# Optimization experiments

Hardware: AMD Instinct MI355X
Metric: run time of the kernel (lower is better)

Reference implementation:

```python
import jax, jax.numpy as jnp
import numpy as np


def _maxpool2(t):
    # 2x2x2 max pool, stride 2. t: [B, C, D, H, W]
    B, C, D, H, W = t.shape
    return t.reshape(B, C, D // 2, 2, H // 2, 2, W // 2, 2).max(axis=(3, 5, 7))


def setup_inputs() -> dict:
    key = jax.random.key(0)
    ks = jax.random.split(key, 5)
    ch = 64
    B, D, H, W = 2, 32, 32, 32
    x = jax.random.normal(ks[0], (B, ch, D, H, W), dtype=jnp.float32)
    # 1x1x1 conv weights (out_ch, in_ch), Kaiming-ish scale
    w_theta = jax.random.normal(ks[1], (ch // 8, ch), dtype=jnp.float32) / np.sqrt(ch)
    w_phi = jax.random.normal(ks[2], (ch // 8, ch), dtype=jnp.float32) / np.sqrt(ch)
    w_g = jax.random.normal(ks[3], (ch // 2, ch), dtype=jnp.float32) / np.sqrt(ch)
    w_o = jax.random.normal(ks[4], (ch, ch // 2), dtype=jnp.float32) / np.sqrt(ch // 2)
    gamma = jnp.ones((), dtype=jnp.float32)  # original inits at 0; 1 gives nontrivial output
    return {"x": x, "w_theta": w_theta, "w_phi": w_phi, "w_g": w_g, "w_o": w_o, "gamma": gamma}


def reference(x, w_theta, w_phi, w_g, w_o, gamma):
    B, C, D, H, W = x.shape
    N = D * H * W
    M = N // 8
    xf = x.reshape(B, C, N)  # [B, C, N]
    # 1x1x1 convs = channel matmuls
    theta = jnp.einsum('oc,bcn->bon', w_theta, xf)                     # [B, C//8, N]
    phi = _maxpool2(jnp.einsum('oc,bcn->bon', w_phi, xf).reshape(B, C // 8, D, H, W)).reshape(B, C // 8, M)
    g = _maxpool2(jnp.einsum('oc,bcn->bon', w_g, xf).reshape(B, C // 2, D, H, W)).reshape(B, C // 2, M)
    # unscaled attention: softmax over keys (M)
    beta = jax.nn.softmax(jnp.einsum('bcn,bcm->bnm', theta, phi), axis=-1)  # [B, N, M]
    o = jnp.einsum('bcm,bnm->bcn', g, beta)                                 # [B, C//2, N]
    out = gamma * jnp.einsum('oc,bcn->bon', w_o, o).reshape(B, C, D, H, W) + x
    return out
```

## Files before the change

### kernel.cpp

```cpp
#include <hip/hip_runtime.h>
#include <cstdint>
#include <cstddef>

typedef __attribute__((ext_vector_type(4))) short short4v;
typedef __attribute__((ext_vector_type(4))) float float4v;

#define C_IN  64
#define NB    2
#define NPTS  32768
#define MPTS  4096
#define LOG2E 1.44269504088896340736f
#define KT    64
#define NTILE (MPTS / KT)
#define QTILES (NPTS / 32)

__device__ __forceinline__ unsigned short f2bf_rne(float f) {
  unsigned int u = __builtin_bit_cast(unsigned int, f);
  u += 0x7fffu + ((u >> 16) & 1u);
  return (unsigned short)(u >> 16);
}

__device__ __forceinline__ short4v pack_bf16_trunc(float a0, float a1, float a2, float a3) {
  unsigned int u0 = __builtin_amdgcn_perm(__builtin_bit_cast(unsigned int, a1),
                                          __builtin_bit_cast(unsigned int, a0), 0x07060302u);
  unsigned int u1 = __builtin_amdgcn_perm(__builtin_bit_cast(unsigned int, a3),
                                          __builtin_bit_cast(unsigned int, a2), 0x07060302u);
  union { unsigned int u[2]; short4v s; } r;
  r.u[0] = u0; r.u[1] = u1;
  return r.s;
}

__device__ __forceinline__ short4v pack_bf16_rne(float a0, float a1, float a2, float a3) {
  short4v s;
  s[0] = (short)f2bf_rne(a0); s[1] = (short)f2bf_rne(a1);
  s[2] = (short)f2bf_rne(a2); s[3] = (short)f2bf_rne(a3);
  return s;
}

__device__ __forceinline__ void gl_lds16(const unsigned short* g, unsigned short* l) {
  __builtin_amdgcn_global_load_lds(
      (const __attribute__((address_space(1))) void*)g,
      (__attribute__((address_space(3))) void*)l, 16, 0, 0);
}


__device__ void pool_body(int idx, const float* __restrict__ x,
                          const float* __restrict__ w_phi,
                          const float* __restrict__ w_g,
                          unsigned short* __restrict__ phi_f,
                          unsigned short* __restrict__ g_f) {
  int b = idx >> 15;
  int rem = idx & 32767;
  int m = rem >> 3, pos = rem & 7;
  int md = m >> 8, mh = (m >> 4) & 15, mw = m & 15;
  int dd = pos >> 2, hh = (pos >> 1) & 1, ww = pos & 1;
  int n = (md * 2 + dd) * 1024 + (mh * 2 + hh) * 32 + (mw * 2 + ww);
  const float* xb = x + (size_t)b * C_IN * NPTS + n;

  float acc[40];
#pragma unroll
  for (int o = 0; o < 40; ++o) acc[o] = 0.f;

#pragma unroll 4
  for (int cc = 0; cc < C_IN; ++cc) {
    float xv = xb[(size_t)cc * NPTS];
#pragma unroll
    for (int o = 0; o < 8; ++o)  acc[o] = fmaf(w_phi[o * C_IN + cc], xv, acc[o]);
#pragma unroll
    for (int o = 0; o < 32; ++o) acc[8 + o] = fmaf(w_g[o * C_IN + cc], xv, acc[8 + o]);
  }

#pragma unroll
  for (int o = 0; o < 40; ++o) {
    float v = acc[o];
    v = fmaxf(v, __shfl_xor(v, 1, 64));
    v = fmaxf(v, __shfl_xor(v, 2, 64));
    v = fmaxf(v, __shfl_xor(v, 4, 64));
    acc[o] = v;
  }

  if (pos == 0) {
    int kt16 = m >> 4, kr = m & 15;
    size_t fb = ((size_t)b * 256 + kt16) * 256;
#pragma unroll
    for (int g2 = 0; g2 < 2; ++g2) {
      unsigned int u0 = (unsigned int)f2bf_rne(acc[g2 * 4 + 0] * LOG2E)
                      | ((unsigned int)f2bf_rne(acc[g2 * 4 + 1] * LOG2E) << 16);
      unsigned int u1 = (unsigned int)f2bf_rne(acc[g2 * 4 + 2] * LOG2E)
                      | ((unsigned int)f2bf_rne(acc[g2 * 4 + 3] * LOG2E) << 16);
      *(uint2*)&phi_f[fb + (g2 * 16 + kr) * 4] = make_uint2(u0, u1);
    }
#pragma unroll
    for (int g2 = 2; g2 < 4; ++g2) {
      *(uint2*)&phi_f[fb + (g2 * 16 + kr) * 4] = make_uint2(0u, 0u);
    }
#pragma unroll
    for (int o = 0; o < 32; ++o) {
      int half = o >> 4, c15 = o & 15;
      size_t base = (((size_t)b * 256 + kt16) * 2 + half) * 256;
      g_f[base + ((kr >> 2) * 16 + c15) * 4 + (kr & 3)] = f2bf_rne(acc[8 + o]);
    }
  }
}

__device__ void theta_body(int idx, const float* __restrict__ x,
                           const float* __restrict__ w_theta,
                           unsigned short* __restrict__ theta_pad) {
  int b = idx >> 15, n = idx & 32767;
  const float* xb = x + (size_t)b * C_IN * NPTS + n;
  float t[8];
#pragma unroll
  for (int o = 0; o < 8; ++o) t[o] = 0.f;
#pragma unroll 4
  for (int cc = 0; cc < C_IN; ++cc) {
    float xv = xb[(size_t)cc * NPTS];
#pragma unroll
    for (int o = 0; o < 8; ++o) t[o] = fmaf(w_theta[o * C_IN + cc], xv, t[o]);
  }
  unsigned int w0 = (unsigned int)f2bf_rne(t[0]) | ((unsigned int)f2bf_rne(t[1]) << 16);
  unsigned int w1 = (unsigned int)f2bf_rne(t[2]) | ((unsigned int)f2bf_rne(t[3]) << 16);
  unsigned int w2 = (unsigned int)f2bf_rne(t[4]) | ((unsigned int)f2bf_rne(t[5]) << 16);
  unsigned int w3 = (unsigned int)f2bf_rne(t[6]) | ((unsigned int)f2bf_rne(t[7]) << 16);
  uint4* dst = (uint4*)(theta_pad + ((size_t)idx << 4));
  dst[0] = make_uint4(w0, w1, w2, w3);
  dst[1] = make_uint4(0u, 0u, 0u, 0u);
}

__global__ __launch_bounds__(256) void prep_fused(
    const float* __restrict__ x, const float* __restrict__ w_theta,
    const float* __restrict__ w_phi, const float* __restrict__ w_g,
    unsigned short* __restrict__ theta_pad,
    unsigned short* __restrict__ phi_f,
    unsigned short* __restrict__ g_f) {
  int gb = blockIdx.x;
  if (gb < 256) {
    pool_body(gb * 256 + threadIdx.x, x, w_phi, w_g, phi_f, g_f);
  } else {
    theta_body((gb - 256) * 256 + threadIdx.x, x, w_theta, theta_pad);
  }
}

template <int KS>
__global__ __launch_bounds__(256) void attn_split_nl(
    const unsigned short* __restrict__ theta_pad,
    const unsigned short* __restrict__ phi_f,
    const unsigned short* __restrict__ g_f,
    float4v* __restrict__ opart,
    float* __restrict__ lbuf) {
  int tid = threadIdx.x;
  int wid = tid >> 6, lane = tid & 63;
  int l4 = lane >> 4, col = lane & 15;
  int b = blockIdx.y / KS;
  int ks = blockIdx.y % KS;
  int qb = blockIdx.x * 128 + wid * 32;

  const unsigned short* tb = theta_pad + ((size_t)(b * NPTS + qb) << 4) + l4 * 4;
  short4v bt0 = *(const short4v*)(tb + (col << 4));
  short4v bt1 = *(const short4v*)(tb + ((16 + col) << 4));

  const int FPB = 256 / KS;
  int f0 = ks * FPB;
  const unsigned short* pp = phi_f + (size_t)b * 65536 + (size_t)f0 * 256 + lane * 4;
  const unsigned short* gp = g_f + (size_t)b * 131072 + (size_t)f0 * 512 + lane * 4;

  float4v acc00 = {0.f, 0.f, 0.f, 0.f}, acc01 = acc00, acc10 = acc00, acc11 = acc00;
  float lsum0 = 0.f, lsum1 = 0.f;

#pragma unroll 4
  for (int f = 0; f < FPB; ++f) {
    short4v pf = *(const short4v*)(pp + (size_t)f * 256);
    short4v g0 = *(const short4v*)(gp + (size_t)f * 512);
    short4v g1 = *(const short4v*)(gp + (size_t)f * 512 + 256);

    float4v zero4 = {0.f, 0.f, 0.f, 0.f};
    float4v s0 = __builtin_amdgcn_mfma_f32_16x16x16bf16_1k(pf, bt0, zero4, 0, 0, 0);
    float4v s1 = __builtin_amdgcn_mfma_f32_16x16x16bf16_1k(pf, bt1, zero4, 0, 0, 0);

    float p00 = __builtin_amdgcn_exp2f(s0[0]);
    float p01 = __builtin_amdgcn_exp2f(s0[1]);
    float p02 = __builtin_amdgcn_exp2f(s0[2]);
    float p03 = __builtin_amdgcn_exp2f(s0[3]);
    float p10 = __builtin_amdgcn_exp2f(s1[0]);
    float p11 = __builtin_amdgcn_exp2f(s1[1]);
    float p12 = __builtin_amdgcn_exp2f(s1[2]);
    float p13 = __builtin_amdgcn_exp2f(s1[3]);
    lsum0 += (p00 + p01) + (p02 + p03);
    lsum1 += (p10 + p11) + (p12 + p13);
    short4v pb0 = pack_bf16_trunc(p00, p01, p02, p03);
    short4v pb1 = pack_bf16_trunc(p10, p11, p12, p13);

    acc00 = __builtin_amdgcn_mfma_f32_16x16x16bf16_1k(g0, pb0, acc00, 0, 0, 0);
    acc01 = __builtin_amdgcn_mfma_f32_16x16x16bf16_1k(g0, pb1, acc01, 0, 0, 0);
    acc10 = __builtin_amdgcn_mfma_f32_16x16x16bf16_1k(g1, pb0, acc10, 0, 0, 0);
    acc11 = __builtin_amdgcn_mfma_f32_16x16x16bf16_1k(g1, pb1, acc11, 0, 0, 0);
  }

  lsum0 += __shfl_xor(lsum0, 16, 64);
  lsum0 += __shfl_xor(lsum0, 32, 64);
  lsum1 += __shfl_xor(lsum1, 16, 64);
  lsum1 += __shfl_xor(lsum1, 32, 64);

  int qt = blockIdx.x * 4 + wid;
  size_t obase = (((size_t)(b * KS + ks) * QTILES + qt) * 4) * 64 + lane;
  opart[obase + 0 * 64] = acc00;
  opart[obase + 1 * 64] = acc01;
  opart[obase + 2 * 64] = acc10;
  opart[obase + 3 * 64] = acc11;
  if (lane < 32) {
    lbuf[((size_t)(b * KS + ks) * QTILES + qt) * 32 + lane] =
        (lane < 16) ? lsum0 : lsum1;
  }
}

template <int KS>
__global__ __launch_bounds__(256) void attn_combine(
    const float* __restrict__ x, const float* __restrict__ w_o,
    const float* __restrict__ gamma_p,
    const float4v* __restrict__ opart,
    const float* __restrict__ lbuf,
    float* __restrict__ out) {
  int tid = threadIdx.x;
  int wid = tid >> 6, lane = tid & 63;
  int l4 = lane >> 4, col = lane & 15;
  int b = blockIdx.y;
  int qt = blockIdx.x * 4 + wid;
  int qb = qt * 32;

  float gamma = gamma_p[0];

  short4v wo[4][2];
#pragma unroll
  for (int cot = 0; cot < 4; ++cot)
#pragma unroll
    for (int ksw = 0; ksw < 2; ++ksw) {
      const float* wp = w_o + (cot * 16 + col) * 32 + ksw * 16 + l4 * 4;
      wo[cot][ksw] = pack_bf16_rne(wp[0] * gamma, wp[1] * gamma,
                                   wp[2] * gamma, wp[3] * gamma);
    }

  float4v a0 = {0.f, 0.f, 0.f, 0.f}, a1 = a0, a2 = a0, a3 = a0;
  float ls0 = 0.f, ls1 = 0.f;
#pragma unroll
  for (int ks = 0; ks < KS; ++ks) {
    size_t ob = (((size_t)(b * KS + ks) * QTILES + qt) * 4) * 64 + lane;
    a0 += opart[ob + 0 * 64];
    a1 += opart[ob + 1 * 64];
    a2 += opart[ob + 2 * 64];
    a3 += opart[ob + 3 * 64];
    const float* lb = lbuf + ((size_t)(b * KS + ks) * QTILES + qt) * 32;
    ls0 += lb[col];
    ls1 += lb[col + 16];
  }
  float li0 = 1.0f / ls0;
  float li1 = 1.0f / ls1;

  short4v onb00 = pack_bf16_rne(a0[0] * li0, a0[1] * li0, a0[2] * li0, a0[3] * li0);
  short4v onb01 = pack_bf16_rne(a1[0] * li1, a1[1] * li1, a1[2] * li1, a1[3] * li1);
  short4v onb10 = pack_bf16_rne(a2[0] * li0, a2[1] * li0, a2[2] * li0, a2[3] * li0);
  short4v onb11 = pack_bf16_rne(a3[0] * li1, a3[1] * li1, a3[2] * li1, a3[3] * li1);

  float4v zero4 = {0.f, 0.f, 0.f, 0.f};
#pragma unroll
  for (int cot = 0; cot < 4; ++cot) {
#pragma unroll
    for (int nt = 0; nt < 2; ++nt) {
      short4v bfrag0 = nt ? onb01 : onb00;
      short4v bfrag1 = nt ? onb11 : onb10;
      float4v d = __builtin_amdgcn_mfma_f32_16x16x16bf16_1k(wo[cot][0], bfrag0, zero4, 0, 0, 0);
      d = __builtin_amdgcn_mfma_f32_16x16x16bf16_1k(wo[cot][1], bfrag1, d, 0, 0, 0);
      int n = qb + nt * 16 + col;
      size_t base = (size_t)(b * C_IN + cot * 16 + l4 * 4) * NPTS + n;
      const float* xp = x + base;
      float* op = out + base;
#pragma unroll
      for (int e = 0; e < 4; ++e) {
        op[(size_t)e * NPTS] = d[e] + xp[(size_t)e * NPTS];
      }
    }
  }
}

__global__ __launch_bounds__(256) void attn_mfma(
    const float* __restrict__ x, const float* __restrict__ w_o,
    const float* __restrict__ gamma_p,
    const unsigned short* __restrict__ theta_pad,
    const unsigned short* __restrict__ phi_f,
    const unsigned short* __restrict__ g_f,
    float* __restrict__ out) {
  __shared__ unsigned short s_phi[2][KT * 16];
  __shared__ unsigned short s_g[2][(KT / 16) * 512];

  int tid = threadIdx.x;
  int wid = tid >> 6, lane = tid & 63;
  int l4 = lane >> 4, col = lane & 15;
  int b = blockIdx.y;
  int qb = blockIdx.x * 128 + wid * 32;

  float gamma = gamma_p[0];

  const unsigned short* tb = theta_pad + ((size_t)(b * NPTS + qb) << 4) + l4 * 4;
  short4v bt0 = *(const short4v*)(tb + (col << 4));
  short4v bt1 = *(const short4v*)(tb + ((16 + col) << 4));

  short4v wo[4][2];
#pragma unroll
  for (int cot = 0; cot < 4; ++cot)
#pragma unroll
    for (int ksw = 0; ksw < 2; ++ksw) {
      const float* wp = w_o + (cot * 16 + col) * 32 + ksw * 16 + l4 * 4;
      wo[cot][ksw] = pack_bf16_rne(wp[0] * gamma, wp[1] * gamma,
                                   wp[2] * gamma, wp[3] * gamma);
    }

  const unsigned short* phib = phi_f + (size_t)b * 256 * 256;
  const unsigned short* gb   = g_f + (size_t)b * 256 * 512;

  float4v acc00 = {0.f, 0.f, 0.f, 0.f}, acc01 = acc00, acc10 = acc00, acc11 = acc00;
  float lsum0 = 0.f, lsum1 = 0.f;

  gl_lds16(gb + 0 * 2048 + wid * 512 + lane * 8, &s_g[0][wid * 512]);
  if (wid < 2)
    gl_lds16(phib + 0 * 1024 + wid * 512 + lane * 8, &s_phi[0][wid * 512]);
  __syncthreads();

#pragma unroll 1
  for (int t = 0; t < NTILE; ++t) {
    int cur = t & 1;
    if (t + 1 < NTILE) {
      gl_lds16(gb + (size_t)(t + 1) * 2048 + wid * 512 + lane * 8,
               &s_g[cur ^ 1][wid * 512]);
      if (wid < 2)
        gl_lds16(phib + (size_t)(t + 1) * 1024 + wid * 512 + lane * 8,
                 &s_phi[cur ^ 1][wid * 512]);
    }
#pragma unroll
    for (int st = 0; st < 4; ++st) {
      short4v pf = *(const short4v*)&s_phi[cur][st * 256 + lane * 4];
      short4v g0 = *(const short4v*)&s_g[cur][st * 512 + lane * 4];
      short4v g1 = *(const short4v*)&s_g[cur][st * 512 + 256 + lane * 4];

      float4v zero4 = {0.f, 0.f, 0.f, 0.f};
      float4v s0 = __builtin_amdgcn_mfma_f32_16x16x16bf16_1k(pf, bt0, zero4, 0, 0, 0);
      float4v s1 = __builtin_amdgcn_mfma_f32_16x16x16bf16_1k(pf, bt1, zero4, 0, 0, 0);

      float p00 = __builtin_amdgcn_exp2f(s0[0]);
      float p01 = __builtin_amdgcn_exp2f(s0[1]);
      float p02 = __builtin_amdgcn_exp2f(s0[2]);
      float p03 = __builtin_amdgcn_exp2f(s0[3]);
      float p10 = __builtin_amdgcn_exp2f(s1[0]);
      float p11 = __builtin_amdgcn_exp2f(s1[1]);
      float p12 = __builtin_amdgcn_exp2f(s1[2]);
      float p13 = __builtin_amdgcn_exp2f(s1[3]);
      lsum0 += (p00 + p01) + (p02 + p03);
      lsum1 += (p10 + p11) + (p12 + p13);
      short4v pb0 = pack_bf16_trunc(p00, p01, p02, p03);
      short4v pb1 = pack_bf16_trunc(p10, p11, p12, p13);

      acc00 = __builtin_amdgcn_mfma_f32_16x16x16bf16_1k(g0, pb0, acc00, 0, 0, 0);
      acc01 = __builtin_amdgcn_mfma_f32_16x16x16bf16_1k(g0, pb1, acc01, 0, 0, 0);
      acc10 = __builtin_amdgcn_mfma_f32_16x16x16bf16_1k(g1, pb0, acc10, 0, 0, 0);
      acc11 = __builtin_amdgcn_mfma_f32_16x16x16bf16_1k(g1, pb1, acc11, 0, 0, 0);
    }
    __syncthreads();
  }

  lsum0 += __shfl_xor(lsum0, 16, 64);
  lsum0 += __shfl_xor(lsum0, 32, 64);
  lsum1 += __shfl_xor(lsum1, 16, 64);
  lsum1 += __shfl_xor(lsum1, 32, 64);
  float li0 = 1.0f / lsum0;
  float li1 = 1.0f / lsum1;

  short4v onb00 = pack_bf16_rne(acc00[0] * li0, acc00[1] * li0, acc00[2] * li0, acc00[3] * li0);
  short4v onb01 = pack_bf16_rne(acc01[0] * li1, acc01[1] * li1, acc01[2] * li1, acc01[3] * li1);
  short4v onb10 = pack_bf16_rne(acc10[0] * li0, acc10[1] * li0, acc10[2] * li0, acc10[3] * li0);
  short4v onb11 = pack_bf16_rne(acc11[0] * li1, acc11[1] * li1, acc11[2] * li1, acc11[3] * li1);

  float4v zero4 = {0.f, 0.f, 0.f, 0.f};
#pragma unroll
  for (int cot = 0; cot < 4; ++cot) {
#pragma unroll
    for (int nt = 0; nt < 2; ++nt) {
      short4v bfrag0 = nt ? onb01 : onb00;
      short4v bfrag1 = nt ? onb11 : onb10;
      float4v d = __builtin_amdgcn_mfma_f32_16x16x16bf16_1k(wo[cot][0], bfrag0, zero4, 0, 0, 0);
      d = __builtin_amdgcn_mfma_f32_16x16x16bf16_1k(wo[cot][1], bfrag1, d, 0, 0, 0);
      int n = qb + nt * 16 + col;
      size_t base = (size_t)(b * C_IN + cot * 16 + l4 * 4) * NPTS + n;
      const float* xp = x + base;
      float* op = out + base;
#pragma unroll
      for (int e = 0; e < 4; ++e) {
        op[(size_t)e * NPTS] = d[e] + xp[(size_t)e * NPTS];
      }
    }
  }
}

extern "C" void kernel_launch(void* const* d_in, const int* in_sizes, int n_in,
                              void* d_out, int out_size, void* d_ws, size_t ws_size,
                              hipStream_t stream) {
  const float* x       = (const float*)d_in[0];
  const float* w_theta = (const float*)d_in[1];
  const float* w_phi   = (const float*)d_in[2];
  const float* w_g     = (const float*)d_in[3];
  const float* w_o     = (const float*)d_in[4];
  const float* gamma   = (const float*)d_in[5];
  float* out = (float*)d_out;

  char* ws = (char*)d_ws;
  unsigned short* theta_pad = (unsigned short*)ws;  ws += (size_t)NB * NPTS * 16 * 2;
  unsigned short* phi_f     = (unsigned short*)ws;  ws += (size_t)NB * 256 * 256 * 2;
  unsigned short* g_f       = (unsigned short*)ws;  ws += (size_t)NB * 256 * 512 * 2;
  size_t base_need = (size_t)(ws - (char*)d_ws);
  float4v* opart = (float4v*)ws;
  size_t opart2 = (size_t)NB * 2 * QTILES * 4 * 64 * sizeof(float4v);
  size_t lbuf2  = (size_t)NB * 2 * QTILES * 32 * sizeof(float);
  size_t need2 = base_need + opart2 + lbuf2;

  prep_fused<<<dim3(512), dim3(256), 0, stream>>>(
      x, w_theta, w_phi, w_g, theta_pad, phi_f, g_f);

  if (ws_size >= need2) {
    float* lbuf = (float*)((char*)opart + opart2);
    attn_split_nl<2><<<dim3(NPTS / 128, NB * 2), dim3(256), 0, stream>>>(
        theta_pad, phi_f, g_f, opart, lbuf);
    attn_combine<2><<<dim3(NPTS / 128, NB), dim3(256), 0, stream>>>(
        x, w_o, gamma, opart, lbuf, out);
  } else if (ws_size >= base_need) {
    attn_mfma<<<dim3(NPTS / 128, NB), dim3(256), 0, stream>>>(
        x, w_o, gamma, theta_pad, phi_f, g_f, out);
  }
}
```

Measured before the change: 98.20 us.

## Fuse theta projection into attention kernel via MFMA and raise key split to four

Drops the separate theta projection pass and its padded bf16 workspace. Each attention wave now computes its own theta fragments with MFMA directly from x and w_theta. The phi/g pooling kernel is restructured so each thread handles one pooled output and four channels, loading the 2x2x2 neighbourhood with float2 loads instead of shuffle reductions. The key split factor goes from 2 to 4 with higher occupancy bounds when workspace allows, adding parallelism at the cost of a larger partial-output combine. Theta is now computed from bf16-rounded x and weights, which lowers precision, and the combine step has more partial outputs to merge.

Result: faster. 95.17 us (-3.1%).

```diff
diff --git a/kernel.cpp b/kernel.cpp
--- a/kernel.cpp
+++ b/kernel.cpp
@@ -44,68 +44,78 @@
 }
 
 
-__device__ void pool_body(int idx, const float* __restrict__ x,
-                          const float* __restrict__ w_phi,
-                          const float* __restrict__ w_g,
-                          unsigned short* __restrict__ phi_f,
-                          unsigned short* __restrict__ g_f) {
-  int b = idx >> 15;
-  int rem = idx & 32767;
-  int m = rem >> 3, pos = rem & 7;
+__global__ __launch_bounds__(256) void pool_proj(
+    const float* __restrict__ x, const float* __restrict__ w_phi,
+    const float* __restrict__ w_g,
+    unsigned short* __restrict__ phi_f,
+    unsigned short* __restrict__ g_f) {
+  int idx = blockIdx.x * 256 + threadIdx.x;
+  int cg = idx >> 13;
+  int bm = idx & 8191;
+  int b = bm >> 12, m = bm & 4095;
   int md = m >> 8, mh = (m >> 4) & 15, mw = m & 15;
-  int dd = pos >> 2, hh = (pos >> 1) & 1, ww = pos & 1;
-  int n = (md * 2 + dd) * 1024 + (mh * 2 + hh) * 32 + (mw * 2 + ww);
-  const float* xb = x + (size_t)b * C_IN * NPTS + n;
-
-  float acc[40];
-#pragma unroll
-  for (int o = 0; o < 40; ++o) acc[o] = 0.f;
+  const float* xb = x + (size_t)b * C_IN * NPTS
+                  + ((md * 2) * 1024 + (mh * 2) * 32 + (mw * 2));
+  const float* wbase = (cg < 2) ? (w_phi + cg * 4 * C_IN)
+                                : (w_g + (cg - 2) * 4 * C_IN);
+
+  float acc[4][8];
+#pragma unroll
+  for (int o = 0; o < 4; ++o)
+#pragma unroll
+    for (int p = 0; p < 8; ++p) acc[o][p] = 0.f;
 
 #pragma unroll 4
   for (int cc = 0; cc < C_IN; ++cc) {
-    float xv = xb[(size_t)cc * NPTS];
-#pragma unroll
-    for (int o = 0; o < 8; ++o)  acc[o] = fmaf(w_phi[o * C_IN + cc], xv, acc[o]);
-#pragma unroll
-    for (int o = 0; o < 32; ++o) acc[8 + o] = fmaf(w_g[o * C_IN + cc], xv, acc[8 + o]);
-  }
-
-#pragma unroll
-  for (int o = 0; o < 40; ++o) {
-    float v = acc[o];
-    v = fmaxf(v, __shfl_xor(v, 1, 64));
-    v = fmaxf(v, __shfl_xor(v, 2, 64));
-    v = fmaxf(v, __shfl_xor(v, 4, 64));
-    acc[o] = v;
-  }
-
-  if (pos == 0) {
-    int kt16 = m >> 4, kr = m & 15;
+    const float* xp = xb + (size_t)cc * NPTS;
+    float2 p01 = *(const float2*)(xp + 0);
+    float2 p23 = *(const float2*)(xp + 32);
+    float2 p45 = *(const float2*)(xp + 1024);
+    float2 p67 = *(const float2*)(xp + 1056);
+#pragma unroll
+    for (int o = 0; o < 4; ++o) {
+      float wv = wbase[o * C_IN + cc];
+      acc[o][0] = fmaf(wv, p01.x, acc[o][0]);
+      acc[o][1] = fmaf(wv, p01.y, acc[o][1]);
+      acc[o][2] = fmaf(wv, p23.x, acc[o][2]);
+      acc[o][3] = fmaf(wv, p23.y, acc[o][3]);
+      acc[o][4] = fmaf(wv, p45.x, acc[o][4]);
+      acc[o][5] = fmaf(wv, p45.y, acc[o][5]);
+      acc[o][6] = fmaf(wv, p67.x, acc[o][6]);
+      acc[o][7] = fmaf(wv, p67.y, acc[o][7]);
+    }
+  }
+  float mx[4];
+#pragma unroll
+  for (int o = 0; o < 4; ++o) {
+    mx[o] = fmaxf(fmaxf(fmaxf(acc[o][0], acc[o][1]), fmaxf(acc[o][2], acc[o][3])),
+                  fmaxf(fmaxf(acc[o][4], acc[o][5]), fmaxf(acc[o][6], acc[o][7])));
+  }
+  int kt16 = m >> 4, kr = m & 15;
+  if (cg < 2) {
     size_t fb = ((size_t)b * 256 + kt16) * 256;
-#pragma unroll
-    for (int g2 = 0; g2 < 2; ++g2) {
-      unsigned int u0 = (unsigned int)f2bf_rne(acc[g2 * 4 + 0] * LOG2E)
-                      | ((unsigned int)f2bf_rne(acc[g2 * 4 + 1] * LOG2E) << 16);
-      unsigned int u1 = (unsigned int)f2bf_rne(acc[g2 * 4 + 2] * LOG2E)
-                      | ((unsigned int)f2bf_rne(acc[g2 * 4 + 3] * LOG2E) << 16);
-      *(uint2*)&phi_f[fb + (g2 * 16 + kr) * 4] = make_uint2(u0, u1);
-    }
-#pragma unroll
-    for (int g2 = 2; g2 < 4; ++g2) {
-      *(uint2*)&phi_f[fb + (g2 * 16 + kr) * 4] = make_uint2(0u, 0u);
-    }
-#pragma unroll
-    for (int o = 0; o < 32; ++o) {
-      int half = o >> 4, c15 = o & 15;
+    unsigned int u0 = (unsigned int)f2bf_rne(mx[0] * LOG2E)
+                    | ((unsigned int)f2bf_rne(mx[1] * LOG2E) << 16);
+    unsigned int u1 = (unsigned int)f2bf_rne(mx[2] * LOG2E)
+                    | ((unsigned int)f2bf_rne(mx[3] * LOG2E) << 16);
+    *(uint2*)&phi_f[fb + (cg * 16 + kr) * 4] = make_uint2(u0, u1);
+    *(uint2*)&phi_f[fb + ((cg + 2) * 16 + kr) * 4] = make_uint2(0u, 0u);
+  } else {
+    int gc0 = (cg - 2) * 4;
+#pragma unroll
+    for (int o = 0; o < 4; ++o) {
+      int c = gc0 + o;
+      int half = c >> 4, c15 = c & 15;
       size_t base = (((size_t)b * 256 + kt16) * 2 + half) * 256;
-      g_f[base + ((kr >> 2) * 16 + c15) * 4 + (kr & 3)] = f2bf_rne(acc[8 + o]);
-    }
-  }
-}
-
-__device__ void theta_body(int idx, const float* __restrict__ x,
-                           const float* __restrict__ w_theta,
-                           unsigned short* __restrict__ theta_pad) {
+      g_f[base + ((kr >> 2) * 16 + c15) * 4 + (kr & 3)] = f2bf_rne(mx[o]);
+    }
+  }
+}
+
+__global__ __launch_bounds__(256) void theta_proj(
+    const float* __restrict__ x, const float* __restrict__ w_theta,
+    unsigned short* __restrict__ theta_pad) {
+  int idx = blockIdx.x * 256 + threadIdx.x;
   int b = idx >> 15, n = idx & 32767;
   const float* xb = x + (size_t)b * C_IN * NPTS + n;
   float t[8];
@@ -126,23 +136,10 @@
   dst[1] = make_uint4(0u, 0u, 0u, 0u);
 }
 
-__global__ __launch_bounds__(256) void prep_fused(
-    const float* __restrict__ x, const float* __restrict__ w_theta,
-    const float* __restrict__ w_phi, const float* __restrict__ w_g,
-    unsigned short* __restrict__ theta_pad,
-    unsigned short* __restrict__ phi_f,
-    unsigned short* __restrict__ g_f) {
-  int gb = blockIdx.x;
-  if (gb < 256) {
-    pool_body(gb * 256 + threadIdx.x, x, w_phi, w_g, phi_f, g_f);
-  } else {
-    theta_body((gb - 256) * 256 + threadIdx.x, x, w_theta, theta_pad);
-  }
-}
-
 template <int KS>
-__global__ __launch_bounds__(256) void attn_split_nl(
-    const unsigned short* __restrict__ theta_pad,
+__global__ __launch_bounds__(256, 8) void attn_split_nl(
+    const float* __restrict__ x,
+    const float* __restrict__ w_theta,
     const unsigned short* __restrict__ phi_f,
     const unsigned short* __restrict__ g_f,
     float4v* __restrict__ opart,
@@ -154,9 +151,21 @@
   int ks = blockIdx.y % KS;
   int qb = blockIdx.x * 128 + wid * 32;
 
-  const unsigned short* tb = theta_pad + ((size_t)(b * NPTS + qb) << 4) + l4 * 4;
-  short4v bt0 = *(const short4v*)(tb + (col << 4));
-  short4v bt1 = *(const short4v*)(tb + ((16 + col) << 4));
+  float4v th0 = {0.f, 0.f, 0.f, 0.f}, th1 = th0;
+#pragma unroll
+  for (int kk = 0; kk < 4; ++kk) {
+    const float* wp = w_theta + (col & 7) * C_IN + kk * 16 + l4 * 4;
+    short4v af = pack_bf16_rne(wp[0], wp[1], wp[2], wp[3]);
+    if (col >= 8) af = (short4v){0, 0, 0, 0};
+    const float* xq = x + (size_t)b * C_IN * NPTS
+                    + (size_t)(kk * 16 + l4 * 4) * NPTS + qb + col;
+    short4v bf0 = pack_bf16_rne(xq[0], xq[NPTS], xq[2 * NPTS], xq[3 * NPTS]);
+    short4v bf1 = pack_bf16_rne(xq[16], xq[NPTS + 16], xq[2 * NPTS + 16], xq[3 * NPTS + 16]);
+    th0 = __builtin_amdgcn_mfma_f32_16x16x16bf16_1k(af, bf0, th0, 0, 0, 0);
+    th1 = __builtin_amdgcn_mfma_f32_16x16x16bf16_1k(af, bf1, th1, 0, 0, 0);
+  }
+  short4v bt0 = pack_bf16_rne(th0[0], th0[1], th0[2], th0[3]);
+  short4v bt1 = pack_bf16_rne(th1[0], th1[1], th1[2], th1[3]);
 
   const int FPB = 256 / KS;
   int f0 = ks * FPB;
@@ -409,25 +418,35 @@
   float* out = (float*)d_out;
 
   char* ws = (char*)d_ws;
-  unsigned short* theta_pad = (unsigned short*)ws;  ws += (size_t)NB * NPTS * 16 * 2;
-  unsigned short* phi_f     = (unsigned short*)ws;  ws += (size_t)NB * 256 * 256 * 2;
-  unsigned short* g_f       = (unsigned short*)ws;  ws += (size_t)NB * 256 * 512 * 2;
-  size_t base_need = (size_t)(ws - (char*)d_ws);
+  unsigned short* phi_f = (unsigned short*)ws;  ws += (size_t)NB * 256 * 256 * 2;
+  unsigned short* g_f   = (unsigned short*)ws;  ws += (size_t)NB * 256 * 512 * 2;
+  size_t frag_need = (size_t)(ws - (char*)d_ws);
   float4v* opart = (float4v*)ws;
+  size_t opart4 = (size_t)NB * 4 * QTILES * 4 * 64 * sizeof(float4v);
   size_t opart2 = (size_t)NB * 2 * QTILES * 4 * 64 * sizeof(float4v);
+  size_t lbuf4  = (size_t)NB * 4 * QTILES * 32 * sizeof(float);
   size_t lbuf2  = (size_t)NB * 2 * QTILES * 32 * sizeof(float);
-  size_t need2 = base_need + opart2 + lbuf2;
-
-  prep_fused<<<dim3(512), dim3(256), 0, stream>>>(
-      x, w_theta, w_phi, w_g, theta_pad, phi_f, g_f);
-
-  if (ws_size >= need2) {
+  size_t need4 = frag_need + opart4 + lbuf4;
+  size_t need2 = frag_need + opart2 + lbuf2;
+  size_t need_fb = frag_need + (size_t)NB * NPTS * 16 * 2;
+
+  pool_proj<<<dim3(320), dim3(256), 0, stream>>>(x, w_phi, w_g, phi_f, g_f);
+
+  if (ws_size >= need4) {
+    float* lbuf = (float*)((char*)opart + opart4);
+    attn_split_nl<4><<<dim3(NPTS / 128, NB * 4), dim3(256), 0, stream>>>(
+        x, w_theta, phi_f, g_f, opart, lbuf);
+    attn_combine<4><<<dim3(NPTS / 128, NB), dim3(256), 0, stream>>>(
+        x, w_o, gamma, opart, lbuf, out);
+  } else if (ws_size >= need2) {
     float* lbuf = (float*)((char*)opart + opart2);
     attn_split_nl<2><<<dim3(NPTS / 128, NB * 2), dim3(256), 0, stream>>>(
-        theta_pad, phi_f, g_f, opart, lbuf);
+        x, w_theta, phi_f, g_f, opart, lbuf);
     attn_combine<2><<<dim3(NPTS / 128, NB), dim3(256), 0, stream>>>(
         x, w_o, gamma, opart, lbuf, out);
-  } else if (ws_size >= base_need) {
+  } else if (ws_size >= need_fb) {
+    unsigned short* theta_pad = (unsigned short*)((char*)d_ws + frag_need);
+    theta_proj<<<dim3((NB * NPTS) / 256), dim3(256), 0, stream>>>(x, w_theta, theta_pad);
     attn_mfma<<<dim3(NPTS / 128, NB), dim3(256), 0, stream>>>(
         x, w_o, gamma, theta_pad, phi_f, g_f, out);
   }
```
